# Kernel optimization log

Hardware: AMD Instinct MI355X
Metric: run time of the kernel (lower is better)

The kernel has to match this reference:

```python
import jax, jax.numpy as jnp
import numpy as np

L, E, M, F, P, C, NC = 12, 768, 256, 3072, 16, 3, 1000
IMG = 224
G = IMG // P          # 14 patches per side
NP = G * G            # 196 patches
B = 16


def setup_inputs() -> dict:
    key = jax.random.key(0)
    ks = jax.random.split(key, 10)
    s = 0.02
    return dict(
        x=jax.random.normal(ks[0], (B, C, IMG, IMG), jnp.float32),
        cls_tok=jax.random.normal(ks[1], (1, 1, E), jnp.float32),
        pos_emb=jax.random.normal(ks[2], (1, NP + 1, E), jnp.float32) * s,
        patch_w=jax.random.normal(ks[3], (E, C, P, P), jnp.float32) * s,
        patch_b=jnp.zeros((E,), jnp.float32),
        ln1_g=jnp.ones((L, E), jnp.float32), ln1_b=jnp.zeros((L, E), jnp.float32),
        proj=jax.random.normal(ks[4], (L, M, E), jnp.float32),  # Performer random features (buffer)
        ln2_g=jnp.ones((L, E), jnp.float32), ln2_b=jnp.zeros((L, E), jnp.float32),
        w1=jax.random.normal(ks[5], (L, E, F), jnp.float32) * s, b1=jnp.zeros((L, F), jnp.float32),
        w2=jax.random.normal(ks[6], (L, F, E), jnp.float32) * s, b2=jnp.zeros((L, E), jnp.float32),
        lnf_g=jnp.ones((E,), jnp.float32), lnf_b=jnp.zeros((E,), jnp.float32),
        head_w=jax.random.normal(ks[7], (E, NC), jnp.float32) * s,
        head_b=jnp.zeros((NC,), jnp.float32),
    )


def _ln(x, g, b):
    mu = jnp.mean(x, -1, keepdims=True)
    var = jnp.var(x, -1, keepdims=True)
    return (x - mu) * jax.lax.rsqrt(var + 1e-5) * g + b


def _performer(x, proj):
    # FaVOR+ softmax-kernel linear attention, non-causal, q=k=v=x. x:[B,N,E], proj:[M,E]
    d = x.shape[-1]
    m = proj.shape[0]
    xp = x * (d ** -0.25)                       # data normalizer d^{-1/4}
    logits = jnp.einsum('bne,me->bnm', xp, proj)
    diag = jnp.sum(xp * xp, -1, keepdims=True) * 0.5
    lg = logits - diag
    eps = 1e-4
    q_feat = jnp.exp(lg - jnp.max(lg, -1, keepdims=True)) * (m ** -0.5) + eps  # per-row max (queries)
    k_feat = jnp.exp(lg - jnp.max(lg)) * (m ** -0.5) + eps                     # global max (keys)
    kv = jnp.einsum('bnm,bne->bme', k_feat, x)                                 # [B,M,E]
    den = jnp.einsum('bnm,bm->bn', q_feat, jnp.sum(k_feat, axis=1))
    return jnp.einsum('bnm,bme->bne', q_feat, kv) / den[..., None]


def reference(x, cls_tok, pos_emb, patch_w, patch_b, ln1_g, ln1_b, proj,
              ln2_g, ln2_b, w1, b1, w2, b2, lnf_g, lnf_b, head_w, head_b):
    bsz = x.shape[0]
    # Conv2d(stride=kernel=P) patch embed == extract patches + matmul
    patches = x.reshape(bsz, C, G, P, G, P).transpose(0, 2, 4, 1, 3, 5).reshape(bsz, NP, C * P * P)
    tok = patches @ patch_w.reshape(E, C * P * P).T + patch_b          # [B,196,E]
    h = jnp.concatenate([jnp.broadcast_to(cls_tok, (bsz, 1, E)), tok], axis=1) + pos_emb

    def block(h, p):
        g1, b1_, pr, g2, b2_, W1, B1, W2, B2 = p
        h = h + _performer(_ln(h, g1, b1_), pr)
        m_in = _ln(h, g2, b2_)
        mlp = jax.nn.gelu(m_in @ W1 + B1, approximate=False) @ W2 + B2
        return h + mlp, None

    h, _ = jax.lax.scan(block, h, (ln1_g, ln1_b, proj, ln2_g, ln2_b, w1, b1, w2, b2))
    cls = _ln(h[:, 0], lnf_g, lnf_b)
    return cls @ head_w + head_b
```

## Files before the change

kernel.cpp:

```cpp
#include <hip/hip_runtime.h>
#include <math.h>

#define BSZ   16
#define NTOK  197
#define NPAT  196
#define EDIM  768
#define MDIM  256
#define FDIM  3072
#define NLAY  12
#define NCLS  1000
#define TTOT  (BSZ*NTOK)
#define TPAT  (BSZ*NPAT)
#define XSCALE 0.18995893f

typedef unsigned short ushortT;
typedef short s16x8 __attribute__((ext_vector_type(8)));
typedef float f32x4 __attribute__((ext_vector_type(4)));

__device__ __forceinline__ float4 ld4(const float* p) {
    return *reinterpret_cast<const float4*>(p);
}
__device__ __forceinline__ ushortT f2bf(float f) {
    unsigned u = __builtin_bit_cast(unsigned, f);
    unsigned r = (u + 0x7fff + ((u >> 16) & 1)) >> 16;
    return (ushortT)r;
}
__device__ __forceinline__ void load_lds16(const ushortT* g, ushortT* lds) {
    __builtin_amdgcn_global_load_lds(
        (const __attribute__((address_space(1))) unsigned int*)g,
        (__attribute__((address_space(3))) unsigned int*)lds, 16, 0, 0);
}
__device__ __forceinline__ unsigned fenc(float f) {
    unsigned u = __builtin_bit_cast(unsigned, f);
    return u ^ ((u >> 31) ? 0xFFFFFFFFu : 0x80000000u);
}
__device__ __forceinline__ float fdec(unsigned u) {
    u ^= ((u >> 31) ? 0x80000000u : 0xFFFFFFFFu);
    return __builtin_bit_cast(float, u);
}

__global__ void gather_patches(const float* __restrict__ x, ushortT* __restrict__ patches) {
    int idx = blockIdx.x * 256 + threadIdx.x;
    if (idx >= TPAT * 768) return;
    int k = idx % 768;
    int t = idx / 768;
    int b = t / NPAT, p = t % NPAT;
    int c = k / 256, r = k % 256;
    int p1 = r / 16, p2 = r % 16;
    int g1 = p / 14, g2 = p % 14;
    patches[idx] = f2bf(x[(((size_t)b * 3 + c) * 224 + (g1 * 16 + p1)) * 224 + (g2 * 16 + p2)]);
}

__global__ void assemble_kernel(const float* __restrict__ tok, const float* __restrict__ cls_tok,
                                const float* __restrict__ pos, float* __restrict__ h) {
    int idx = blockIdx.x * 256 + threadIdx.x;
    int e = idx % 768;
    int t = idx / 768;
    int b = t / NTOK, n = t % NTOK;
    float v = (n == 0) ? cls_tok[e] : tok[((size_t)(b * NPAT + n - 1)) * 768 + e];
    h[idx] = v + pos[n * 768 + e];
}

__global__ void cvt_bf16(const float* __restrict__ in, ushortT* __restrict__ out, int n) {
    int idx = blockIdx.x * 256 + threadIdx.x;
    if (idx < n) out[idx] = f2bf(in[idx]);
}

__global__ void init_gmax(unsigned* __restrict__ g) {
    if (threadIdx.x < NLAY) g[threadIdx.x] = 0u;
}

__launch_bounds__(256)
__global__ void transpose_cvt(const float* __restrict__ in, ushortT* __restrict__ out,
                              int R, int Ccol) {
    size_t elems = (size_t)R * Ccol;
    const float* ip = in + (size_t)blockIdx.z * elems;
    ushortT* op = out + (size_t)blockIdx.z * elems;
    __shared__ float tile[32][33];
    int c0 = blockIdx.x * 32, r0 = blockIdx.y * 32;
    int tx = threadIdx.x & 31, ty = threadIdx.x >> 5;
    #pragma unroll
    for (int i = 0; i < 32; i += 8)
        tile[ty + i][tx] = ip[(size_t)(r0 + ty + i) * Ccol + c0 + tx];
    __syncthreads();
    #pragma unroll
    for (int i = 0; i < 32; i += 8)
        op[(size_t)(c0 + ty + i) * R + r0 + tx] = f2bf(tile[tx][ty + i]);
}

template<int EPI>
__launch_bounds__(256)
__global__ void mgemm(const ushortT* __restrict__ A, const ushortT* __restrict__ Bt,
                      const float* __restrict__ bias, float* __restrict__ C,
                      ushortT* __restrict__ Cb, int M, int N, int K) {
    __shared__ ushortT As[128 * 32];
    __shared__ ushortT Bs[128 * 32];
    const int t = threadIdx.x;
    const int n0 = blockIdx.x * 128;
    const int m0 = blockIdx.y * 128;
    const int lane = t & 63;
    const int wv = t >> 6;
    const int wm = (wv >> 1) * 64;
    const int wn = (wv & 1) * 64;
    f32x4 acc[4][4];
    #pragma unroll
    for (int i = 0; i < 4; ++i)
        #pragma unroll
        for (int j = 0; j < 4; ++j) acc[i][j] = (f32x4)0.f;

    const ushortT* aptr = A + (size_t)(m0 + (t >> 2)) * K + (t & 3) * 8;
    const ushortT* bptr = Bt + (size_t)(n0 + (t >> 2)) * K + (t & 3) * 8;
    ushortT* aLds = As + t * 8;
    ushortT* bLds = Bs + t * 8;
    const size_t rowStep = (size_t)64 * K;

    const int fr = lane & 15;
    const int fko = (lane >> 4) * 8;
    const ushortT* aRd = As + (wm + fr) * 32 + fko;
    const ushortT* bRd = Bs + (wn + fr) * 32 + fko;

    for (int k0 = 0; k0 < K; k0 += 32) {
        load_lds16(aptr, aLds);
        load_lds16(aptr + rowStep, aLds + 2048);
        load_lds16(bptr, bLds);
        load_lds16(bptr + rowStep, bLds + 2048);
        aptr += 32; bptr += 32;
        __syncthreads();
        s16x8 af[4], bfr[4];
        #pragma unroll
        for (int i = 0; i < 4; ++i) af[i] = *(const s16x8*)(aRd + i * 512);
        #pragma unroll
        for (int j = 0; j < 4; ++j) bfr[j] = *(const s16x8*)(bRd + j * 512);
        #pragma unroll
        for (int i = 0; i < 4; ++i)
            #pragma unroll
            for (int j = 0; j < 4; ++j)
                acc[i][j] = __builtin_amdgcn_mfma_f32_16x16x32_bf16(af[i], bfr[j], acc[i][j], 0, 0, 0);
        __syncthreads();
    }

    const int orow = (lane >> 4) * 4;
    const int ocol = lane & 15;
    #pragma unroll
    for (int i = 0; i < 4; ++i) {
        #pragma unroll
        for (int r = 0; r < 4; ++r) {
            int row = m0 + wm + i * 16 + orow + r;
            if (row >= M) continue;
            #pragma unroll
            for (int j = 0; j < 4; ++j) {
                int col = n0 + wn + j * 16 + ocol;
                float v = acc[i][j][r] + bias[col];
                size_t o = (size_t)row * N + col;
                if (EPI == 0) {
                    C[o] = v;
                } else {
                    v = 0.5f * v * (1.0f + erff(v * 0.70710678118f));
                    Cb[o] = f2bf(v);
                }
            }
        }
    }
}

__launch_bounds__(256)
__global__ void mgemm64(const ushortT* __restrict__ A, const ushortT* __restrict__ Bt,
                        const float* __restrict__ bias, float* __restrict__ C,
                        int M, int N, int K) {
    __shared__ ushortT As[64 * 32];
    __shared__ ushortT Bs[64 * 32];
    const int t = threadIdx.x;
    const int n0 = blockIdx.x * 64;
    const int m0 = blockIdx.y * 64;
    const int lane = t & 63;
    const int wv = t >> 6;
    const int wm = (wv >> 1) * 32;
    const int wn = (wv & 1) * 32;
    f32x4 acc[2][2];
    #pragma unroll
    for (int i = 0; i < 2; ++i)
        #pragma unroll
        for (int j = 0; j < 2; ++j) acc[i][j] = (f32x4)0.f;

    const ushortT* aptr = A + (size_t)(m0 + (t >> 2)) * K + (t & 3) * 8;
    const ushortT* bptr = Bt + (size_t)(n0 + (t >> 2)) * K + (t & 3) * 8;
    ushortT* aLds = As + t * 8;
    ushortT* bLds = Bs + t * 8;

    const int fr = lane & 15;
    const int fko = (lane >> 4) * 8;
    const ushortT* aRd = As + (wm + fr) * 32 + fko;
    const ushortT* bRd = Bs + (wn + fr) * 32 + fko;

    for (int k0 = 0; k0 < K; k0 += 32) {
        load_lds16(aptr, aLds);
        load_lds16(bptr, bLds);
        aptr += 32; bptr += 32;
        __syncthreads();
        s16x8 af[2], bfr[2];
        #pragma unroll
        for (int i = 0; i < 2; ++i) af[i] = *(const s16x8*)(aRd + i * 512);
        #pragma unroll
        for (int j = 0; j < 2; ++j) bfr[j] = *(const s16x8*)(bRd + j * 512);
        #pragma unroll
        for (int i = 0; i < 2; ++i)
            #pragma unroll
            for (int j = 0; j < 2; ++j)
                acc[i][j] = __builtin_amdgcn_mfma_f32_16x16x32_bf16(af[i], bfr[j], acc[i][j], 0, 0, 0);
        __syncthreads();
    }

    const int orow = (lane >> 4) * 4;
    const int ocol = lane & 15;
    #pragma unroll
    for (int i = 0; i < 2; ++i) {
        #pragma unroll
        for (int r = 0; r < 4; ++r) {
            int row = m0 + wm + i * 16 + orow + r;
            if (row >= M) continue;
            #pragma unroll
            for (int j = 0; j < 2; ++j) {
                int col = n0 + wn + j * 16 + ocol;
                float v = acc[i][j][r] + bias[col];
                size_t o = (size_t)row * N + col;
                C[o] = C[o] + v;
            }
        }
    }
}

__launch_bounds__(256)
__global__ void gemm64_lg(const float* __restrict__ A, const float* __restrict__ Bm,
                          const float* __restrict__ diag, float* __restrict__ Cd,
                          int Mrows, int Ncols, int Kdim) {
    __shared__ float As[16][64];
    __shared__ float Bs[16][64];
    const int tid = threadIdx.x;
    const int n0 = blockIdx.x * 64;
    const int m0 = blockIdx.y * 64;
    const int tx = tid & 15, ty = tid >> 4;
    float acc[4][4] = {};
    const int lr = tid >> 2;
    const int lc = (tid & 3) << 2;
    for (int k0 = 0; k0 < Kdim; k0 += 16) {
        float4 av = make_float4(0.f, 0.f, 0.f, 0.f);
        int ar = m0 + lr;
        if (ar < Mrows) av = ld4(A + (size_t)ar * Kdim + k0 + lc);
        As[lc + 0][lr] = av.x; As[lc + 1][lr] = av.y;
        As[lc + 2][lr] = av.z; As[lc + 3][lr] = av.w;
        int bn = tid >> 2;
        int bk = (tid & 3) << 2;
        float4 bv = ld4(Bm + (size_t)(n0 + bn) * Kdim + k0 + bk);
        Bs[bk + 0][bn] = bv.x; Bs[bk + 1][bn] = bv.y;
        Bs[bk + 2][bn] = bv.z; Bs[bk + 3][bn] = bv.w;
        __syncthreads();
        #pragma unroll
        for (int k = 0; k < 16; ++k) {
            float a[4], bb[4];
            #pragma unroll
            for (int i = 0; i < 4; ++i) a[i] = As[k][ty * 4 + i];
            #pragma unroll
            for (int j = 0; j < 4; ++j) bb[j] = Bs[k][tx * 4 + j];
            #pragma unroll
            for (int i = 0; i < 4; ++i)
                #pragma unroll
                for (int j = 0; j < 4; ++j)
                    acc[i][j] += a[i] * bb[j];
        }
        __syncthreads();
    }
    #pragma unroll
    for (int i = 0; i < 4; ++i) {
        int row = m0 + ty * 4 + i;
        if (row >= Mrows) continue;
        #pragma unroll
        for (int j = 0; j < 4; ++j) {
            int col = n0 + tx * 4 + j;
            Cd[(size_t)row * Ncols + col] = acc[i][j] * XSCALE - diag[row];
        }
    }
}

__launch_bounds__(256)
__global__ void ln_kernel(const float* __restrict__ in, int rowStride,
                          const float* __restrict__ g, const float* __restrict__ b,
                          float* __restrict__ out, ushortT* __restrict__ outb,
                          float* __restrict__ diag) {
    int row = blockIdx.x;
    const float* xr = in + (size_t)row * rowStride;
    int tid = threadIdx.x;
    float v0 = xr[tid], v1 = xr[tid + 256], v2 = xr[tid + 512];
    float s = v0 + v1 + v2;
    float q = v0 * v0 + v1 * v1 + v2 * v2;
    int lane = tid & 63, wid = tid >> 6;
    #pragma unroll
    for (int off = 32; off >= 1; off >>= 1) {
        s += __shfl_down(s, off);
        q += __shfl_down(q, off);
    }
    __shared__ float sh[8];
    __shared__ float mu_s, rs_s;
    if (lane == 0) { sh[wid] = s; sh[4 + wid] = q; }
    __syncthreads();
    if (tid == 0) {
        float ts = sh[0] + sh[1] + sh[2] + sh[3];
        float tq = sh[4] + sh[5] + sh[6] + sh[7];
        float mu = ts * (1.0f / 768.0f);
        float var = tq * (1.0f / 768.0f) - mu * mu;
        mu_s = mu;
        rs_s = rsqrtf(var + 1e-5f);
    }
    __syncthreads();
    float mu = mu_s, rs = rs_s;
    float y0 = (v0 - mu) * rs * g[tid] + b[tid];
    float y1 = (v1 - mu) * rs * g[tid + 256] + b[tid + 256];
    float y2 = (v2 - mu) * rs * g[tid + 512] + b[tid + 512];
    size_t o = (size_t)row * 768;
    out[o + tid] = y0;
    out[o + tid + 256] = y1;
    out[o + tid + 512] = y2;
    if (outb) {
        outb[o + tid] = f2bf(y0);
        outb[o + tid + 256] = f2bf(y1);
        outb[o + tid + 512] = f2bf(y2);
    }
    if (diag) {
        float qq = y0 * y0 + y1 * y1 + y2 * y2;
        #pragma unroll
        for (int off = 32; off >= 1; off >>= 1) qq += __shfl_down(qq, off);
        if (lane == 0) sh[wid] = qq;
        __syncthreads();
        if (tid == 0) diag[row] = 0.5f * XSCALE * XSCALE * (sh[0] + sh[1] + sh[2] + sh[3]);
    }
}

__launch_bounds__(256)
__global__ void rowqf_kernel(const float* __restrict__ lg, float* __restrict__ qf,
                             unsigned* __restrict__ gslot) {
    int row = blockIdx.x;
    int tid = threadIdx.x;
    float v = lg[(size_t)row * 256 + tid];
    float m = v;
    int lane = tid & 63, wid = tid >> 6;
    #pragma unroll
    for (int off = 32; off >= 1; off >>= 1) m = fmaxf(m, __shfl_down(m, off));
    __shared__ float sh[4];
    __shared__ float bm_s;
    if (lane == 0) sh[wid] = m;
    __syncthreads();
    if (tid == 0) {
        float bm = fmaxf(fmaxf(sh[0], sh[1]), fmaxf(sh[2], sh[3]));
        bm_s = bm;
        atomicMax(gslot, fenc(bm));
    }
    __syncthreads();
    qf[(size_t)row * 256 + tid] = expf(v - bm_s) * 0.0625f + 1e-4f;
}

__launch_bounds__(256)
__global__ void kv_kernel(const float* __restrict__ lg, const unsigned* __restrict__ gslot,
                          const float* __restrict__ xln,
                          float* __restrict__ kv, float* __restrict__ ksum) {
    int blk = blockIdx.x;
    int b = blk >> 5;
    int m0 = (blk & 31) << 3;
    __shared__ float kc[NTOK * 8];
    int tid = threadIdx.x;
    float gm = fdec(*gslot);
    for (int i = tid; i < NTOK * 8; i += 256) {
        int n = i >> 3, j = i & 7;
        float lv = lg[((size_t)(b * NTOK + n)) * 256 + m0 + j];
        kc[i] = expf(lv - gm) * 0.0625f + 1e-4f;
    }
    __syncthreads();
    if (tid < 8) {
        float s = 0.f;
        for (int n = 0; n < NTOK; ++n) s += kc[n * 8 + tid];
        ksum[b * 256 + m0 + tid] = s;
    }
    float acc[8][3] = {};
    const float* xb = xln + (size_t)b * NTOK * 768;
    for (int n = 0; n < NTOK; ++n) {
        float x0 = xb[n * 768 + tid];
        float x1 = xb[n * 768 + tid + 256];
        float x2 = xb[n * 768 + tid + 512];
        #pragma unroll
        for (int j = 0; j < 8; ++j) {
            float kk = kc[n * 8 + j];
            acc[j][0] += kk * x0;
            acc[j][1] += kk * x1;
            acc[j][2] += kk * x2;
        }
    }
    float* kvb = kv + ((size_t)b * 256 + m0) * 768;
    #pragma unroll
    for (int j = 0; j < 8; ++j) {
        kvb[j * 768 + tid] = acc[j][0];
        kvb[j * 768 + tid + 256] = acc[j][1];
        kvb[j * 768 + tid + 512] = acc[j][2];
    }
}

__launch_bounds__(256)
__global__ void att_ln2(const float* __restrict__ qf, const float* __restrict__ ksum,
                        const float* __restrict__ kv, float* __restrict__ h,
                        const float* __restrict__ lng, const float* __restrict__ lnb,
                        ushortT* __restrict__ xlnbf) {
    int blk = blockIdx.x;
    int b = blk / 25;
    int n0 = (blk % 25) * 8;
    int nrows = NTOK - n0; if (nrows > 8) nrows = 8;
    __shared__ float qs[8][256];
    __shared__ float dinv[8];
    __shared__ float sh[8];
    __shared__ float mu_s, rs_s;
    int tid = threadIdx.x;
    for (int r = 0; r < nrows; ++r)
        qs[r][tid] = qf[((size_t)(b * NTOK + n0 + r)) * 256 + tid];
    for (int r = nrows; r < 8; ++r) qs[r][tid] = 0.f;
    __syncthreads();
    int lane = tid & 63, wid = tid >> 6;
    float ks = ksum[b * 256 + tid];
    for (int r = 0; r < nrows; ++r) {
        float d = qs[r][tid] * ks;
        #pragma unroll
        for (int off = 32; off >= 1; off >>= 1) d += __shfl_down(d, off);
        if (lane == 0) sh[wid] = d;
        __syncthreads();
        if (tid == 0) dinv[r] = 1.0f / (sh[0] + sh[1] + sh[2] + sh[3]);
        __syncthreads();
    }
    float acc[8][3] = {};
    const float* kvb = kv + (size_t)b * 256 * 768;
    for (int m = 0; m < 256; ++m) {
        float k0 = kvb[m * 768 + tid];
        float k1 = kvb[m * 768 + tid + 256];
        float k2 = kvb[m * 768 + tid + 512];
        #pragma unroll
        for (int r = 0; r < 8; ++r) {
            float qv = qs[r][m];
            acc[r][0] += qv * k0;
            acc[r][1] += qv * k1;
            acc[r][2] += qv * k2;
        }
    }
    float g0 = lng[tid], g1 = lng[tid + 256], g2 = lng[tid + 512];
    float c0 = lnb[tid], c1 = lnb[tid + 256], c2 = lnb[tid + 512];
    for (int r = 0; r < nrows; ++r) {
        float di = dinv[r];
        size_t o = ((size_t)(b * NTOK + n0 + r)) * 768;
        float h0 = h[o + tid]       + acc[r][0] * di;
        float h1 = h[o + tid + 256] + acc[r][1] * di;
        float h2 = h[o + tid + 512] + acc[r][2] * di;
        h[o + tid] = h0; h[o + tid + 256] = h1; h[o + tid + 512] = h2;
        float s = h0 + h1 + h2;
        float q = h0 * h0 + h1 * h1 + h2 * h2;
        #pragma unroll
        for (int off = 32; off >= 1; off >>= 1) {
            s += __shfl_down(s, off);
            q += __shfl_down(q, off);
        }
        if (lane == 0) { sh[wid] = s; sh[4 + wid] = q; }
        __syncthreads();
        if (tid == 0) {
            float ts = sh[0] + sh[1] + sh[2] + sh[3];
            float tq = sh[4] + sh[5] + sh[6] + sh[7];
            float mu = ts * (1.0f / 768.0f);
            mu_s = mu;
            rs_s = rsqrtf(tq * (1.0f / 768.0f) - mu * mu + 1e-5f);
        }
        __syncthreads();
        float mu = mu_s, rs = rs_s;
        xlnbf[o + tid]       = f2bf((h0 - mu) * rs * g0 + c0);
        xlnbf[o + tid + 256] = f2bf((h1 - mu) * rs * g1 + c1);
        xlnbf[o + tid + 512] = f2bf((h2 - mu) * rs * g2 + c2);
    }
}

__global__ void head_kernel(const float* __restrict__ cls, const float* __restrict__ w,
                            const float* __restrict__ hb, float* __restrict__ out) {
    int idx = blockIdx.x * 256 + threadIdx.x;
    if (idx >= BSZ * NCLS) return;
    int i = idx / NCLS, j = idx % NCLS;
    float acc = hb[j];
    const float* cr = cls + (size_t)i * 768;
    for (int k = 0; k < 768; ++k) acc += cr[k] * w[k * NCLS + j];
    out[idx] = acc;
}

extern "C" void kernel_launch(void* const* d_in, const int* in_sizes, int n_in,
                              void* d_out, int out_size, void* d_ws, size_t ws_size,
                              hipStream_t stream) {
    const float* x       = (const float*)d_in[0];
    const float* cls_tok = (const float*)d_in[1];
    const float* pos_emb = (const float*)d_in[2];
    const float* patch_w = (const float*)d_in[3];
    const float* patch_b = (const float*)d_in[4];
    const float* ln1_g   = (const float*)d_in[5];
    const float* ln1_b   = (const float*)d_in[6];
    const float* proj    = (const float*)d_in[7];
    const float* ln2_g   = (const float*)d_in[8];
    const float* ln2_b   = (const float*)d_in[9];
    const float* w1      = (const float*)d_in[10];
    const float* b1      = (const float*)d_in[11];
    const float* w2      = (const float*)d_in[12];
    const float* b2      = (const float*)d_in[13];
    const float* lnf_g   = (const float*)d_in[14];
    const float* lnf_b   = (const float*)d_in[15];
    const float* head_w  = (const float*)d_in[16];
    const float* head_b  = (const float*)d_in[17];
    float* out = (float*)d_out;

    char* wsb = (char*)d_ws;
    ushortT* y1b        = (ushortT*)wsb;
    float*   tok        = (float*)wsb;
    ushortT* patches_bf = (ushortT*)(wsb + 9633792);
    size_t off = 19660800;
    float*    h      = (float*)(wsb + off);    off += 9682944;
    float*    xln    = (float*)(wsb + off);    off += 9830400;
    ushortT*  xln_bf = (ushortT*)(wsb + off);  off += 4915200;
    float*    lg     = (float*)(wsb + off);    off += 3227648;
    float*    qf     = (float*)(wsb + off);    off += 3227648;
    float*    kv     = (float*)(wsb + off);    off += 12582912;
    ushortT*  pwb    = (ushortT*)(wsb + off);  off += 1179648;
    float*    diag   = (float*)(wsb + off);    off += 12800;
    unsigned* gml    = (unsigned*)(wsb + off); off += 256;
    float*    ksum   = (float*)(wsb + off);    off += 16384;
    float*    clsln  = (float*)(wsb + off);    off += 49152;
    const size_t WSTRIDE = (size_t)3072 * 768;
    ushortT*  w1t    = (ushortT*)(wsb + off);
    bool big = ws_size >= off + 2u * NLAY * WSTRIDE * sizeof(ushortT);
    size_t w1bytes = (big ? NLAY : 1) * WSTRIDE * sizeof(ushortT);
    ushortT*  w2t    = (ushortT*)(wsb + off + w1bytes);

    init_gmax<<<1, 64, 0, stream>>>(gml);

    if (big) {
        transpose_cvt<<<dim3(96, 24, NLAY), 256, 0, stream>>>(w1, w1t, 768, FDIM);
        transpose_cvt<<<dim3(24, 96, NLAY), 256, 0, stream>>>(w2, w2t, FDIM, 768);
    }

    gather_patches<<<9408, 256, 0, stream>>>(x, patches_bf);
    cvt_bf16<<<2304, 256, 0, stream>>>(patch_w, pwb, 768 * 768);
    mgemm<0><<<dim3(6, 25), 256, 0, stream>>>(patches_bf, pwb, patch_b, tok, nullptr,
                                              TPAT, 768, 768);
    assemble_kernel<<<9456, 256, 0, stream>>>(tok, cls_tok, pos_emb, h);

    for (int l = 0; l < NLAY; ++l) {
        ushortT* w1l = big ? w1t + (size_t)l * WSTRIDE : w1t;
        ushortT* w2l = big ? w2t + (size_t)l * WSTRIDE : w2t;
        if (!big) {
            transpose_cvt<<<dim3(96, 24), 256, 0, stream>>>(w1 + (size_t)l * WSTRIDE, w1l, 768, FDIM);
            transpose_cvt<<<dim3(24, 96), 256, 0, stream>>>(w2 + (size_t)l * WSTRIDE, w2l, FDIM, 768);
        }

        ln_kernel<<<TTOT, 256, 0, stream>>>(h, 768, ln1_g + l * 768, ln1_b + l * 768,
                                            xln, nullptr, diag);
        gemm64_lg<<<dim3(4, 50), 256, 0, stream>>>(xln, proj + (size_t)l * 256 * 768,
                                                   diag, lg, TTOT, 256, 768);
        rowqf_kernel<<<TTOT, 256, 0, stream>>>(lg, qf, gml + l);
        kv_kernel<<<BSZ * 32, 256, 0, stream>>>(lg, gml + l, xln, kv, ksum);
        att_ln2<<<BSZ * 25, 256, 0, stream>>>(qf, ksum, kv, h,
                                              ln2_g + l * 768, ln2_b + l * 768, xln_bf);
        mgemm<1><<<dim3(24, 25), 256, 0, stream>>>(xln_bf, w1l, b1 + l * FDIM,
                                                   nullptr, y1b, TTOT, FDIM, 768);
        mgemm64<<<dim3(12, 50), 256, 0, stream>>>(y1b, w2l, b2 + l * 768,
                                                  h, TTOT, 768, FDIM);
    }

    ln_kernel<<<BSZ, 256, 0, stream>>>(h, NTOK * 768, lnf_g, lnf_b, clsln, nullptr, nullptr);
    head_kernel<<<(BSZ * NCLS + 255) / 256, 256, 0, stream>>>(clsln, head_w, head_b, out);
}
```

Baseline: 3.690 ms.

## Move Performer projection GEMM to bf16 MFMA and batch att_ln2 reductions

Replaces the fp32 SIMT logits GEMM with the bf16 MFMA 64x64 GEMM, using a new epilogue mode that applies the scale and diagonal subtraction. Projection weights are converted to bf16 once, and the LayerNorm now also emits bf16 activations. The patch-embed GEMM moves to the 64x64 tile for more blocks. att_ln2 replaces per-row barrier reductions with batched reductions across all 8 rows, cutting syncthreads. Risks: bf16 logits feed exp with a global max, which lowers precision. The final LN also writes into xln_bf, a buffer that is not used afterwards.

```diff
diff --git a/kernel.cpp b/kernel.cpp
--- a/kernel.cpp
+++ b/kernel.cpp
@@ -88,11 +88,10 @@
         op[(size_t)(c0 + ty + i) * R + r0 + tx] = f2bf(tile[tx][ty + i]);
 }
 
-template<int EPI>
-__launch_bounds__(256)
-__global__ void mgemm(const ushortT* __restrict__ A, const ushortT* __restrict__ Bt,
-                      const float* __restrict__ bias, float* __restrict__ C,
-                      ushortT* __restrict__ Cb, int M, int N, int K) {
+__launch_bounds__(256)
+__global__ void mgemm128_gelu(const ushortT* __restrict__ A, const ushortT* __restrict__ Bt,
+                              const float* __restrict__ bias, ushortT* __restrict__ Cb,
+                              int M, int N, int K) {
     __shared__ ushortT As[128 * 32];
     __shared__ ushortT Bs[128 * 32];
     const int t = threadIdx.x;
@@ -151,22 +150,18 @@
             for (int j = 0; j < 4; ++j) {
                 int col = n0 + wn + j * 16 + ocol;
                 float v = acc[i][j][r] + bias[col];
-                size_t o = (size_t)row * N + col;
-                if (EPI == 0) {
-                    C[o] = v;
-                } else {
-                    v = 0.5f * v * (1.0f + erff(v * 0.70710678118f));
-                    Cb[o] = f2bf(v);
-                }
+                v = 0.5f * v * (1.0f + erff(v * 0.70710678118f));
+                Cb[(size_t)row * N + col] = f2bf(v);
             }
         }
     }
 }
 
+template<int EPI>
 __launch_bounds__(256)
 __global__ void mgemm64(const ushortT* __restrict__ A, const ushortT* __restrict__ Bt,
-                        const float* __restrict__ bias, float* __restrict__ C,
-                        int M, int N, int K) {
+                        const float* __restrict__ bias, const float* __restrict__ diag,
+                        float* __restrict__ C, int M, int N, int K) {
     __shared__ ushortT As[64 * 32];
     __shared__ ushortT Bs[64 * 32];
     const int t = threadIdx.x;
@@ -221,62 +216,16 @@
             #pragma unroll
             for (int j = 0; j < 2; ++j) {
                 int col = n0 + wn + j * 16 + ocol;
-                float v = acc[i][j][r] + bias[col];
+                float v = acc[i][j][r];
                 size_t o = (size_t)row * N + col;
-                C[o] = C[o] + v;
+                if (EPI == 0) {
+                    C[o] = v + bias[col];
+                } else if (EPI == 2) {
+                    C[o] = C[o] + v + bias[col];
+                } else {
+                    C[o] = v * XSCALE - diag[row];
+                }
             }
-        }
-    }
-}
-
-__launch_bounds__(256)
-__global__ void gemm64_lg(const float* __restrict__ A, const float* __restrict__ Bm,
-                          const float* __restrict__ diag, float* __restrict__ Cd,
-                          int Mrows, int Ncols, int Kdim) {
-    __shared__ float As[16][64];
-    __shared__ float Bs[16][64];
-    const int tid = threadIdx.x;
-    const int n0 = blockIdx.x * 64;
-    const int m0 = blockIdx.y * 64;
-    const int tx = tid & 15, ty = tid >> 4;
-    float acc[4][4] = {};
-    const int lr = tid >> 2;
-    const int lc = (tid & 3) << 2;
-    for (int k0 = 0; k0 < Kdim; k0 += 16) {
-        float4 av = make_float4(0.f, 0.f, 0.f, 0.f);
-        int ar = m0 + lr;
-        if (ar < Mrows) av = ld4(A + (size_t)ar * Kdim + k0 + lc);
-        As[lc + 0][lr] = av.x; As[lc + 1][lr] = av.y;
-        As[lc + 2][lr] = av.z; As[lc + 3][lr] = av.w;
-        int bn = tid >> 2;
-        int bk = (tid & 3) << 2;
-        float4 bv = ld4(Bm + (size_t)(n0 + bn) * Kdim + k0 + bk);
-        Bs[bk + 0][bn] = bv.x; Bs[bk + 1][bn] = bv.y;
-        Bs[bk + 2][bn] = bv.z; Bs[bk + 3][bn] = bv.w;
-        __syncthreads();
-        #pragma unroll
-        for (int k = 0; k < 16; ++k) {
-            float a[4], bb[4];
-            #pragma unroll
-            for (int i = 0; i < 4; ++i) a[i] = As[k][ty * 4 + i];
-            #pragma unroll
-            for (int j = 0; j < 4; ++j) bb[j] = Bs[k][tx * 4 + j];
-            #pragma unroll
-            for (int i = 0; i < 4; ++i)
-                #pragma unroll
-                for (int j = 0; j < 4; ++j)
-                    acc[i][j] += a[i] * bb[j];
-        }
-        __syncthreads();
-    }
-    #pragma unroll
-    for (int i = 0; i < 4; ++i) {
-        int row = m0 + ty * 4 + i;
-        if (row >= Mrows) continue;
-        #pragma unroll
-        for (int j = 0; j < 4; ++j) {
-            int col = n0 + tx * 4 + j;
-            Cd[(size_t)row * Ncols + col] = acc[i][j] * XSCALE - diag[row];
         }
     }
 }
@@ -411,25 +360,30 @@
     int n0 = (blk % 25) * 8;
     int nrows = NTOK - n0; if (nrows > 8) nrows = 8;
     __shared__ float qs[8][256];
+    __shared__ float redA[8][4];
+    __shared__ float redB[8][4];
     __shared__ float dinv[8];
-    __shared__ float sh[8];
-    __shared__ float mu_s, rs_s;
+    __shared__ float mu8[8], rs8[8];
     int tid = threadIdx.x;
-    for (int r = 0; r < nrows; ++r)
-        qs[r][tid] = qf[((size_t)(b * NTOK + n0 + r)) * 256 + tid];
-    for (int r = nrows; r < 8; ++r) qs[r][tid] = 0.f;
-    __syncthreads();
     int lane = tid & 63, wid = tid >> 6;
+    #pragma unroll
+    for (int r = 0; r < 8; ++r)
+        qs[r][tid] = (r < nrows) ? qf[((size_t)(b * NTOK + n0 + r)) * 256 + tid] : 0.f;
+    __syncthreads();
     float ks = ksum[b * 256 + tid];
-    for (int r = 0; r < nrows; ++r) {
+    #pragma unroll
+    for (int r = 0; r < 8; ++r) {
         float d = qs[r][tid] * ks;
         #pragma unroll
         for (int off = 32; off >= 1; off >>= 1) d += __shfl_down(d, off);
-        if (lane == 0) sh[wid] = d;
-        __syncthreads();
-        if (tid == 0) dinv[r] = 1.0f / (sh[0] + sh[1] + sh[2] + sh[3]);
-        __syncthreads();
-    }
+        if (lane == 0) redA[r][wid] = d;
+    }
+    __syncthreads();
+    if (tid < 8) {
+        float d = redA[tid][0] + redA[tid][1] + redA[tid][2] + redA[tid][3];
+        dinv[tid] = 1.0f / d;
+    }
+    __syncthreads();
     float acc[8][3] = {};
     const float* kvb = kv + (size_t)b * 256 * 768;
     for (int m = 0; m < 256; ++m) {
@@ -444,36 +398,45 @@
             acc[r][2] += qv * k2;
         }
     }
+    float hv[8][3];
+    #pragma unroll
+    for (int r = 0; r < 8; ++r) {
+        float ps = 0.f, pq = 0.f;
+        if (r < nrows) {
+            float di = dinv[r];
+            size_t o = ((size_t)(b * NTOK + n0 + r)) * 768;
+            float h0 = h[o + tid]       + acc[r][0] * di;
+            float h1 = h[o + tid + 256] + acc[r][1] * di;
+            float h2 = h[o + tid + 512] + acc[r][2] * di;
+            h[o + tid] = h0; h[o + tid + 256] = h1; h[o + tid + 512] = h2;
+            hv[r][0] = h0; hv[r][1] = h1; hv[r][2] = h2;
+            ps = h0 + h1 + h2;
+            pq = h0 * h0 + h1 * h1 + h2 * h2;
+        }
+        #pragma unroll
+        for (int off = 32; off >= 1; off >>= 1) {
+            ps += __shfl_down(ps, off);
+            pq += __shfl_down(pq, off);
+        }
+        if (lane == 0) { redA[r][wid] = ps; redB[r][wid] = pq; }
+    }
+    __syncthreads();
+    if (tid < 8) {
+        float ts = redA[tid][0] + redA[tid][1] + redA[tid][2] + redA[tid][3];
+        float tq = redB[tid][0] + redB[tid][1] + redB[tid][2] + redB[tid][3];
+        float mu = ts * (1.0f / 768.0f);
+        mu8[tid] = mu;
+        rs8[tid] = rsqrtf(tq * (1.0f / 768.0f) - mu * mu + 1e-5f);
+    }
+    __syncthreads();
     float g0 = lng[tid], g1 = lng[tid + 256], g2 = lng[tid + 512];
     float c0 = lnb[tid], c1 = lnb[tid + 256], c2 = lnb[tid + 512];
     for (int r = 0; r < nrows; ++r) {
-        float di = dinv[r];
+        float mu = mu8[r], rs = rs8[r];
         size_t o = ((size_t)(b * NTOK + n0 + r)) * 768;
-        float h0 = h[o + tid]       + acc[r][0] * di;
-        float h1 = h[o + tid + 256] + acc[r][1] * di;
-        float h2 = h[o + tid + 512] + acc[r][2] * di;
-        h[o + tid] = h0; h[o + tid + 256] = h1; h[o + tid + 512] = h2;
-        float s = h0 + h1 + h2;
-        float q = h0 * h0 + h1 * h1 + h2 * h2;
-        #pragma unroll
-        for (int off = 32; off >= 1; off >>= 1) {
-            s += __shfl_down(s, off);
-            q += __shfl_down(q, off);
-        }
-        if (lane == 0) { sh[wid] = s; sh[4 + wid] = q; }
-        __syncthreads();
-        if (tid == 0) {
-            float ts = sh[0] + sh[1] + sh[2] + sh[3];
-            float tq = sh[4] + sh[5] + sh[6] + sh[7];
-            float mu = ts * (1.0f / 768.0f);
-            mu_s = mu;
-            rs_s = rsqrtf(tq * (1.0f / 768.0f) - mu * mu + 1e-5f);
-        }
-        __syncthreads();
-        float mu = mu_s, rs = rs_s;
-        xlnbf[o + tid]       = f2bf((h0 - mu) * rs * g0 + c0);
-        xlnbf[o + tid + 256] = f2bf((h1 - mu) * rs * g1 + c1);
-        xlnbf[o + tid + 512] = f2bf((h2 - mu) * rs * g2 + c2);
+        xlnbf[o + tid]       = f2bf((hv[r][0] - mu) * rs * g0 + c0);
+        xlnbf[o + tid + 256] = f2bf((hv[r][1] - mu) * rs * g1 + c1);
+        xlnbf[o + tid + 512] = f2bf((hv[r][2] - mu) * rs * g2 + c2);
     }
 }
 
@@ -523,6 +486,7 @@
     float*    qf     = (float*)(wsb + off);    off += 3227648;
     float*    kv     = (float*)(wsb + off);    off += 12582912;
     ushortT*  pwb    = (ushortT*)(wsb + off);  off += 1179648;
+    ushortT*  projb  = (ushortT*)(wsb + off);  off += 4718592;
     float*    diag   = (float*)(wsb + off);    off += 12800;
     unsigned* gml    = (unsigned*)(wsb + off); off += 256;
     float*    ksum   = (float*)(wsb + off);    off += 16384;
@@ -539,11 +503,12 @@
         transpose_cvt<<<dim3(96, 24, NLAY), 256, 0, stream>>>(w1, w1t, 768, FDIM);
         transpose_cvt<<<dim3(24, 96, NLAY), 256, 0, stream>>>(w2, w2t, FDIM, 768);
     }
+    cvt_bf16<<<(NLAY * MDIM * EDIM + 255) / 256, 256, 0, stream>>>(proj, projb, NLAY * MDIM * EDIM);
 
     gather_patches<<<9408, 256, 0, stream>>>(x, patches_bf);
     cvt_bf16<<<2304, 256, 0, stream>>>(patch_w, pwb, 768 * 768);
-    mgemm<0><<<dim3(6, 25), 256, 0, stream>>>(patches_bf, pwb, patch_b, tok, nullptr,
-                                              TPAT, 768, 768);
+    mgemm64<0><<<dim3(12, 49), 256, 0, stream>>>(patches_bf, pwb, patch_b, nullptr, tok,
+                                                 TPAT, 768, 768);
     assemble_kernel<<<9456, 256, 0, stream>>>(tok, cls_tok, pos_emb, h);
 
     for (int l = 0; l < NLAY; ++l) {
@@ -555,19 +520,19 @@
         }
 
         ln_kernel<<<TTOT, 256, 0, stream>>>(h, 768, ln1_g + l * 768, ln1_b + l * 768,
-                                            xln, nullptr, diag);
-        gemm64_lg<<<dim3(4, 50), 256, 0, stream>>>(xln, proj + (size_t)l * 256 * 768,
-                                                   diag, lg, TTOT, 256, 768);
+                                            xln, xln_bf, diag);
+        mgemm64<3><<<dim3(4, 50), 256, 0, stream>>>(xln_bf, projb + (size_t)l * MDIM * EDIM,
+                                                    nullptr, diag, lg, TTOT, 256, 768);
         rowqf_kernel<<<TTOT, 256, 0, stream>>>(lg, qf, gml + l);
         kv_kernel<<<BSZ * 32, 256, 0, stream>>>(lg, gml + l, xln, kv, ksum);
         att_ln2<<<BSZ * 25, 256, 0, stream>>>(qf, ksum, kv, h,
                                               ln2_g + l * 768, ln2_b + l * 768, xln_bf);
-        mgemm<1><<<dim3(24, 25), 256, 0, stream>>>(xln_bf, w1l, b1 + l * FDIM,
-                                                   nullptr, y1b, TTOT, FDIM, 768);
-        mgemm64<<<dim3(12, 50), 256, 0, stream>>>(y1b, w2l, b2 + l * 768,
-                                                  h, TTOT, 768, FDIM);
-    }
-
-    ln_kernel<<<BSZ, 256, 0, stream>>>(h, NTOK * 768, lnf_g, lnf_b, clsln, nullptr, nullptr);
+        mgemm128_gelu<<<dim3(24, 25), 256, 0, stream>>>(xln_bf, w1l, b1 + l * FDIM,
+                                                        y1b, TTOT, FDIM, 768);
+        mgemm64<2><<<dim3(12, 50), 256, 0, stream>>>(y1b, w2l, b2 + l * 768, nullptr,
+                                                     h, TTOT, 768, FDIM);
+    }
+
+    ln_kernel<<<BSZ, 256, 0, stream>>>(h, NTOK * 768, lnf_g, lnf_b, clsln, xln_bf, nullptr);
     head_kernel<<<(BSZ * NCLS + 255) / 256, 256, 0, stream>>>(clsln, head_w, head_b, out);
 }
```

After: 3.186 ms. 13.7% less time.
